# Performance work log

Measured on AMD Instinct MI355X. Metric: run time of the kernel, lower is better.

## Reference

```python
import jax, jax.numpy as jnp
import numpy as np

B, S, E = 512, 200, 128
NUM_C = 1024
DIFF = 100


def _glorot(k, shape):
    fan_in, fan_out = shape[-1], shape[0]
    lim = jnp.sqrt(6.0 / (fan_in + fan_out)).astype(jnp.float32)
    return jax.random.uniform(k, shape, jnp.float32, -lim, lim)


def setup_inputs() -> dict:
    key = jax.random.key(0)
    ks = jax.random.split(key, 16)
    c = jax.random.randint(ks[0], (B, S), 0, NUM_C + 1)
    sd = jax.random.randint(ks[1], (B, S), 0, DIFF + 2)
    a = jax.random.randint(ks[2], (B, S), 0, 2)
    cshft = jax.random.randint(ks[3], (B, S), 0, NUM_C + 1)
    sdshft = jax.random.randint(ks[4], (B, S), 0, DIFF + 2)
    # embedding tables (padding_idx=0 rows zeroed, as in nn.Embedding)
    c_table = _glorot(ks[5], (NUM_C + 1, E)).at[0].set(0.0)
    sd_table = _glorot(ks[6], (DIFF + 2, E)).at[0].set(0.0)
    a_table = _glorot(ks[7], (2, E))
    knowledge = _glorot(ks[8], (1, E))  # xavier_uniform [1, E]
    W1 = _glorot(ks[9], (E, 2 * E)); b1 = jnp.zeros((E,), jnp.float32)
    W2 = _glorot(ks[10], (E, E));     b2 = jnp.zeros((E,), jnp.float32)
    W3 = _glorot(ks[11], (E, E));     b3 = jnp.zeros((E,), jnp.float32)
    W4 = _glorot(ks[12], (E, 2 * E)); b4 = jnp.zeros((E,), jnp.float32)
    W5 = _glorot(ks[13], (E, 2 * E)); b5 = jnp.zeros((E,), jnp.float32)
    W6 = _glorot(ks[14], (E, 3 * E)); b6 = jnp.zeros((E,), jnp.float32)
    return dict(c=c, sd=sd, a=a, cshft=cshft, sdshft=sdshft,
                c_table=c_table, sd_table=sd_table, a_table=a_table,
                knowledge=knowledge,
                W1=W1, b1=b1, W2=W2, b2=b2, W3=W3, b3=b3,
                W4=W4, b4=b4, W5=W5, b5=b5, W6=W6, b6=b6)


def reference(c, sd, a, cshft, sdshft, c_table, sd_table, a_table, knowledge,
              W1, b1, W2, b2, W3, b3, W4, b4, W5, b5, W6, b6):
    # embedding lookups: [B, S, E]
    c_emb = c_table[c]
    sd_emb = sd_table[sd]
    a_emb = a_table[a]
    target_c = c_table[cshft]
    target_sd = sd_table[sdshft]

    input_data = jnp.concatenate((c_emb, sd_emb), -1) @ W1.T + b1      # [B,S,E]
    target_data = jnp.concatenate((target_c, target_sd), -1) @ W1.T + b1

    k0 = jnp.broadcast_to(knowledge, (c.shape[0], knowledge.shape[-1]))  # [B,E]

    def step(k, xs):
        sd_t, a_t, in_t = xs                       # each [B,E]
        qq = k - in_t
        gates_SDF = jax.nn.sigmoid(qq @ W2.T + b2)
        SDFt = gates_SDF * jnp.tanh(qq @ W3.T + b3)  # dropout = eval-mode identity
        x = jnp.concatenate((SDFt, a_t), -1)
        gates_PKA = jax.nn.sigmoid(x @ W4.T + b4)
        PKAt = gates_PKA * jnp.tanh(x @ W5.T + b5)
        ins = jnp.concatenate((k, a_t, sd_t), -1)
        gates_KSU = jax.nn.sigmoid(ins @ W6.T + b6)
        k_new = gates_KSU * k + (1.0 - gates_KSU) * PKAt
        return k_new, k_new

    xs = (jnp.swapaxes(sd_emb, 0, 1),      # [S,B,E]
          jnp.swapaxes(a_emb, 0, 1),
          jnp.swapaxes(input_data, 0, 1))
    _, hs = jax.lax.scan(step, k0, xs)     # hs: [S,B,E]
    output = jnp.swapaxes(hs, 0, 1)        # [B,S,E]

    logits = jnp.sum(target_data * output, axis=-1)  # [B,S]
    return jax.nn.sigmoid(logits)
```

## Files before the change

### kernel.cpp

```cpp
#include <hip/hip_runtime.h>


#define S_ 200
#define E_ 128
#define RS 136

typedef float  float4v __attribute__((ext_vector_type(4)));
typedef _Float16 f16x8 __attribute__((ext_vector_type(8)));

#define BAR() asm volatile("s_waitcnt lgkmcnt(0)\n\ts_barrier" ::: "memory")

#define MFMA(A, B, C) __builtin_amdgcn_mfma_f32_16x16x32_f16((A), (B), (C), 0, 0, 0)

__device__ __forceinline__ float fast_sigmoid(float x) {
  return __builtin_amdgcn_rcpf(1.f + __expf(-x));
}
__device__ __forceinline__ float swz16(float x) {
  return __builtin_bit_cast(float,
      __builtin_amdgcn_ds_swizzle(__builtin_bit_cast(int, x), 0x401F));
}

#define DPP_ADD(x, ctrl) \
  ((x) + __builtin_bit_cast(float, __builtin_amdgcn_update_dpp( \
       0, __builtin_bit_cast(int, (x)), (ctrl), 0xf, 0xf, true)))

__device__ __forceinline__ f16x8 cvt8(const float* __restrict__ p) {
  float4v a = *(const float4v*)p;
  float4v b = *(const float4v*)(p + 4);
  f16x8 r;
  r[0] = (_Float16)a[0]; r[1] = (_Float16)a[1];
  r[2] = (_Float16)a[2]; r[3] = (_Float16)a[3];
  r[4] = (_Float16)b[0]; r[5] = (_Float16)b[1];
  r[6] = (_Float16)b[2]; r[7] = (_Float16)b[3];
  return r;
}

__global__ __launch_bounds__(256) void dimkt_prep(
    const float* __restrict__ c_table, const float* __restrict__ sd_table,
    const float* __restrict__ a_table,
    const float* __restrict__ W1, const float* __restrict__ b1,
    const float* __restrict__ W4, const float* __restrict__ b4,
    const float* __restrict__ W5, const float* __restrict__ b5,
    const float* __restrict__ W6, const float* __restrict__ b6,
    float* __restrict__ ws) {
  __shared__ __attribute__((aligned(16))) float s_src[8][E_];
  __shared__ float s_w[E_][33];
  const int blk = blockIdx.x, t = threadIdx.x;
  const int e = t & 127, h = t >> 7;
  const float* src; const float* wb; const float* bias; float* dst;
  int r0, maxrow, wstr, woff, dstr;
  if (blk < 129)      { r0 = blk * 8;       src = c_table;  maxrow = 1024; wb = W1; wstr = 256; woff = 0;   bias = nullptr; dst = ws;          dstr = 128; }
  else if (blk < 142) { r0 = (blk-129) * 8; src = sd_table; maxrow = 101;  wb = W1; wstr = 256; woff = 128; bias = b1;      dst = ws + 131200; dstr = 256; }
  else if (blk < 155) { r0 = (blk-142) * 8; src = sd_table; maxrow = 101;  wb = W6; wstr = 384; woff = 256; bias = nullptr; dst = ws + 131328; dstr = 256; }
  else if (blk == 155){ r0 = 0;             src = a_table;  maxrow = 1;    wb = W4; wstr = 256; woff = 128; bias = b4;      dst = ws + 157312; dstr = 128; }
  else if (blk == 156){ r0 = 0;             src = a_table;  maxrow = 1;    wb = W5; wstr = 256; woff = 128; bias = b5;      dst = ws + 157568; dstr = 128; }
  else                { r0 = 0;             src = a_table;  maxrow = 1;    wb = W6; wstr = 384; woff = 128; bias = b6;      dst = ws + 157824; dstr = 128; }
  #pragma unroll
  for (int i = 0; i < 4; ++i) {
    int idx = i * 256 + t, row = idx >> 7, col = idx & 127;
    int rr = r0 + row; if (rr > maxrow) rr = maxrow;
    s_src[row][col] = src[rr * E_ + col];
  }
  float binit = bias ? bias[e] : 0.f;
  float acc[4] = {binit, binit, binit, binit};
  for (int k0 = 0; k0 < 4; ++k0) {
    __syncthreads();
    #pragma unroll
    for (int i = 0; i < 16; ++i) {
      int idx = i * 256 + t;
      s_w[idx >> 5][idx & 31] = wb[(idx >> 5) * wstr + woff + k0 * 32 + (idx & 31)];
    }
    __syncthreads();
    #pragma unroll 4
    for (int kk = 0; kk < 32; ++kk) {
      float wv = s_w[e][kk];
      #pragma unroll
      for (int g = 0; g < 4; ++g)
        acc[g] += wv * s_src[h * 4 + g][k0 * 32 + kk];
    }
  }
  #pragma unroll
  for (int g = 0; g < 4; ++g) {
    int row = r0 + h * 4 + g;
    if (row <= maxrow) dst[row * dstr + e] = acc[g];
  }
}

__global__ __launch_bounds__(512, 2) void dimkt_scan(
    const int* __restrict__ c, const int* __restrict__ sd, const int* __restrict__ a,
    const int* __restrict__ cshft, const int* __restrict__ sdshft,
    const float* __restrict__ knowledge,
    const float* __restrict__ W2, const float* __restrict__ b2,
    const float* __restrict__ W3, const float* __restrict__ b3,
    const float* __restrict__ W4, const float* __restrict__ W5,
    const float* __restrict__ W6,
    const float* __restrict__ ws, float* __restrict__ out) {

  const float* __restrict__ C1   = ws;
  const float* __restrict__ SD1I = ws + 131200;
  const float* __restrict__ A4  = ws + 157312;
  const float* __restrict__ A5  = ws + 157568;
  const float* __restrict__ A6  = ws + 157824;

  const int tid  = threadIdx.x;
  const int w    = tid >> 6;
  const int lane = tid & 63;
  const int l15  = lane & 15;
  const int q    = lane >> 4;
  const int qodd = q & 1;
  const int e    = w * 16 + l15;
  const int j    = q >> 1;
  const int bj   = blockIdx.x * 2 + j;

  __shared__ __attribute__((aligned(16))) _Float16 A1[16 * RS];
  __shared__ __attribute__((aligned(16))) _Float16 A2[16 * RS];
  __shared__ __attribute__((aligned(32))) int idx_lds[S_ + 2][2][8];
  __shared__ float part[8][2][S_];

  for (int i = tid; i < 2 * (S_ + 2); i += 512) {
    const int jj = (i >= S_ + 2) ? 1 : 0;
    const int ss = jj ? (i - (S_ + 2)) : i;
    const int sc = ss < S_ ? ss : S_ - 1;
    const int src = (blockIdx.x * 2 + jj) * S_ + sc;
    idx_lds[ss][jj][0] = c[src];
    idx_lds[ss][jj][1] = sd[src];
    idx_lds[ss][jj][2] = a[src];
    idx_lds[ss][jj][3] = cshft[src];
    idx_lds[ss][jj][4] = sdshft[src];
  }

  const int stq = (j * 8) * RS + e;
  const int stk = stq + RS;
  const int rd0 = l15 * RS + q * 8;
  const bool m1 = (l15 & 6) == 0;
  const bool m2 = (l15 & 7) == 0;

  f16x8 w2f[4], w3f[4], w4f[4], w5f[4], w6f[4];
  #pragma unroll
  for (int t = 0; t < 4; ++t) {
    const int ko = t * 32 + q * 8;
    w2f[t] = cvt8(W2 + e * 128 + ko);
    w3f[t] = cvt8(W3 + e * 128 + ko);
    w4f[t] = cvt8(W4 + e * 256 + ko);
    w5f[t] = cvt8(W5 + e * 256 + ko);
    w6f[t] = cvt8(W6 + e * 384 + ko);
  }
  const float b2e = b2[e], b3e = b3[e];
  const float A4t0 = A4[e], A4t1 = A4[E_ + e];
  const float A5t0 = A5[e], A5t1 = A5[E_ + e];
  const float A6t0 = A6[e], A6t1 = A6[E_ + e];

  float kreg = knowledge[e];

  const int base = bj * S_;
  int ic = c[base], isd = sd[base], ia = a[base], ict = cshft[base], ist = sdshft[base];
  float inT0 = C1[ic * E_ + e] + SD1I[isd * 256 + e];
  float sd6v = SD1I[isd * 256 + 128 + e];
  float a4v = ia ? A4t1 : A4t0;
  float a5v = ia ? A5t1 : A5t0;
  float a6v = ia ? A6t1 : A6t0;
  float tgt  = C1[ict * E_ + e] + SD1I[ist * 256 + e];
  float sumPrev = tgt;
  int nic = c[base + 1], nisd = sd[base + 1], nia = a[base + 1],
      nict = cshft[base + 1], nist = sdshft[base + 1];

  __syncthreads();
  if (!qodd) {
    A1[stq] = (_Float16)(kreg - inT0);
    A1[stk] = (_Float16)kreg;
  }
  __syncthreads();

  f16x8 f0{}, f1{}, f2{}, f3{};
  f16x8 g0{}, g1{}, g2v{}, g3{};

  const float4v cin2{b2e, 0.f, 0.f, 0.f};
  const float4v cin3{b3e, 0.f, 0.f, 0.f};
  float4v acc6{0.f,0.f,0.f,0.f};
  float4v acc4{0.f,0.f,0.f,0.f}, acc5{0.f,0.f,0.f,0.f};

  float pprev = 0.f;
  int   sprev = 0;

  #pragma unroll 2
  for (int s = 0; s < S_; ++s) {
    if (m1) {
      f0 = *(const f16x8*)&A1[rd0];
      f1 = *(const f16x8*)&A1[rd0 + 32];
      f2 = *(const f16x8*)&A1[rd0 + 64];
      f3 = *(const f16x8*)&A1[rd0 + 96];
    }

    tgt = swz16(sumPrev);

    const int selc  = qodd ? nict : nic;
    const int selsd = qodd ? nist : nisd;
    const float L1 = C1[selc * E_ + e];
    const float* pSD = SD1I + selsd * 256 + e;
    const float L2   = pSD[0];
    const float nsd6 = pSD[128];
    const float na4 = nia ? A4t1 : A4t0;
    const float na5 = nia ? A5t1 : A5t0;
    const float na6 = nia ? A6t1 : A6t0;

    const int4 iv = *(const int4*)&idx_lds[s + 2][j][0];
    const int tist = idx_lds[s + 2][j][4];

    __builtin_amdgcn_s_setprio(1);
    float4v a2 = MFMA(f0, w2f[0], cin2);
    float4v a3 = MFMA(f0, w3f[0], cin3);
    a2 = MFMA(f1, w2f[1], a2);
    a3 = MFMA(f1, w3f[1], a3);
    a2 = MFMA(f2, w2f[2], a2);
    a3 = MFMA(f2, w3f[2], a3);
    a2 = MFMA(f3, w2f[3], a2);
    a3 = MFMA(f3, w3f[3], a3);

    acc6[1] = a6v + sd6v;
    acc6 = MFMA(f0, w6f[0], acc6);
    acc6 = MFMA(f1, w6f[1], acc6);

    const float g2  = fast_sigmoid(a2[0]);
    const float G2  = g2 + g2;
    const float sg3 = __builtin_amdgcn_rcpf(1.f + __expf(-2.f * a3[0]));
    const float sdfv = G2 * sg3 - g2;
    if (!qodd) A2[stq] = (_Float16)sdfv;

    acc6 = MFMA(f2, w6f[2], acc6);
    acc6 = MFMA(f3, w6f[3], acc6);
    __builtin_amdgcn_s_setprio(0);

    BAR();

    if (m2) {
      g0  = *(const f16x8*)&A2[rd0];
      g1  = *(const f16x8*)&A2[rd0 + 32];
      g2v = *(const f16x8*)&A2[rd0 + 64];
      g3  = *(const f16x8*)&A2[rd0 + 96];
    }

    const float g6 = fast_sigmoid(acc6[1]);
    const float gk = g6 * kreg;
    const float h6 = 1.f - g6;

    if (s > 0) {
      float pr = pprev;
      pr = DPP_ADD(pr, 0x111);
      pr = DPP_ADD(pr, 0x112);
      pr = DPP_ADD(pr, 0x114);
      pr = DPP_ADD(pr, 0x118);
      if (l15 == 15 && !qodd) part[w][j][sprev] = pr;
    }

    __builtin_amdgcn_s_setprio(1);
    acc4[0] = a4v;
    acc4 = MFMA(g0, w4f[0], acc4);
    acc4 = MFMA(g1, w4f[1], acc4);
    acc4 = MFMA(g2v, w4f[2], acc4);
    acc4 = MFMA(g3, w4f[3], acc4);
    acc5[0] = a5v;
    acc5 = MFMA(g0, w5f[0], acc5);
    acc5 = MFMA(g1, w5f[1], acc5);

    const float s4  = fast_sigmoid(acc4[0]);
    const float S42 = s4 + s4;

    acc5 = MFMA(g2v, w5f[2], acc5);
    acc5 = MFMA(g3, w5f[3], acc5);
    __builtin_amdgcn_s_setprio(0);

    const float sg5 = __builtin_amdgcn_rcpf(1.f + __expf(-2.f * acc5[0]));
    const float pka = S42 * sg5 - s4;
    const float knew = pka * h6 + gk;
    kreg = knew;

    const float sum = L1 + L2;

    if (!qodd) {
      A1[stq] = (_Float16)(knew - sum);
      A1[stk] = (_Float16)knew;
    }

    pprev = tgt * knew;
    sprev = s;

    sumPrev = sum;
    sd6v = nsd6; a4v = na4; a5v = na5; a6v = na6;
    nic = iv.x; nisd = iv.y; nia = iv.z; nict = iv.w; nist = tist;

    BAR();
  }

  {
    float pr = pprev;
    pr = DPP_ADD(pr, 0x111);
    pr = DPP_ADD(pr, 0x112);
    pr = DPP_ADD(pr, 0x114);
    pr = DPP_ADD(pr, 0x118);
    if (l15 == 15 && !qodd) part[w][j][sprev] = pr;
  }

  __syncthreads();
  for (int i = tid; i < 2 * S_; i += 512) {
    const int jj = (i >= S_) ? 1 : 0;
    const int ss = jj ? (i - S_) : i;
    float logit = 0.f;
    #pragma unroll
    for (int x = 0; x < 8; ++x) logit += part[x][jj][ss];
    out[(blockIdx.x * 2 + jj) * S_ + ss] = fast_sigmoid(logit);
  }
}

extern "C" void kernel_launch(void* const* d_in, const int* in_sizes, int n_in,
                              void* d_out, int out_size, void* d_ws, size_t ws_size,
                              hipStream_t stream) {
  const int*   c         = (const int*)  d_in[0];
  const int*   sd        = (const int*)  d_in[1];
  const int*   a         = (const int*)  d_in[2];
  const int*   cshft     = (const int*)  d_in[3];
  const int*   sdshft    = (const int*)  d_in[4];
  const float* c_table   = (const float*)d_in[5];
  const float* sd_table  = (const float*)d_in[6];
  const float* a_table   = (const float*)d_in[7];
  const float* knowledge = (const float*)d_in[8];
  const float* W1 = (const float*)d_in[9];  const float* b1 = (const float*)d_in[10];
  const float* W2 = (const float*)d_in[11]; const float* b2 = (const float*)d_in[12];
  const float* W3 = (const float*)d_in[13]; const float* b3 = (const float*)d_in[14];
  const float* W4 = (const float*)d_in[15]; const float* b4 = (const float*)d_in[16];
  const float* W5 = (const float*)d_in[17]; const float* b5 = (const float*)d_in[18];
  const float* W6 = (const float*)d_in[19]; const float* b6 = (const float*)d_in[20];
  float* ws  = (float*)d_ws;
  float* out = (float*)d_out;
  (void)in_sizes; (void)n_in; (void)out_size; (void)ws_size;

  dimkt_prep<<<158, 256, 0, stream>>>(c_table, sd_table, a_table,
                                      W1, b1, W4, b4, W5, b5, W6, b6, ws);
  dimkt_scan<<<256, 512, 0, stream>>>(c, sd, a, cshft, sdshft, knowledge,
                                      W2, b2, W3, b3, W4, W5, W6, ws, out);
}
```

Baseline: 246.6 us.

## Process one batch row per block with 4 waves each owning 32 output features

The scan kernel now handles one sequence per block with 256 threads instead of two sequences with 512 threads. Each wave covers 32 output features using two MFMA tiles per gate, so it holds twice as many weight fragments in registers. The MFMA A-operand rows are duplicated across both 8-row halves. The grid doubles to 512 blocks, which shortens the per-step barriers to 4 waves and spreads work over more CUs. In exchange, each wave has a longer serial MFMA chain per step, higher register pressure, and redundant MFMA work on duplicated rows.

```diff
diff --git a/kernel.cpp b/kernel.cpp
--- a/kernel.cpp
+++ b/kernel.cpp
@@ -86,7 +86,7 @@
   }
 }
 
-__global__ __launch_bounds__(512, 2) void dimkt_scan(
+__global__ __launch_bounds__(256, 2) void dimkt_scan(
     const int* __restrict__ c, const int* __restrict__ sd, const int* __restrict__ a,
     const int* __restrict__ cshft, const int* __restrict__ sdshft,
     const float* __restrict__ knowledge,
@@ -108,42 +108,44 @@
   const int l15  = lane & 15;
   const int q    = lane >> 4;
   const int qodd = q & 1;
-  const int e    = w * 16 + l15;
-  const int j    = q >> 1;
-  const int bj   = blockIdx.x * 2 + j;
+  const int tt   = lane >> 5;
+  const int et0  = w * 32 + l15;
+  const int e    = et0 + tt * 16;
+  const int bj   = blockIdx.x;
 
   __shared__ __attribute__((aligned(16))) _Float16 A1[16 * RS];
   __shared__ __attribute__((aligned(16))) _Float16 A2[16 * RS];
-  __shared__ __attribute__((aligned(32))) int idx_lds[S_ + 2][2][8];
-  __shared__ float part[8][2][S_];
-
-  for (int i = tid; i < 2 * (S_ + 2); i += 512) {
-    const int jj = (i >= S_ + 2) ? 1 : 0;
-    const int ss = jj ? (i - (S_ + 2)) : i;
-    const int sc = ss < S_ ? ss : S_ - 1;
-    const int src = (blockIdx.x * 2 + jj) * S_ + sc;
-    idx_lds[ss][jj][0] = c[src];
-    idx_lds[ss][jj][1] = sd[src];
-    idx_lds[ss][jj][2] = a[src];
-    idx_lds[ss][jj][3] = cshft[src];
-    idx_lds[ss][jj][4] = sdshft[src];
-  }
-
-  const int stq = (j * 8) * RS + e;
-  const int stk = stq + RS;
+  __shared__ __attribute__((aligned(32))) int idx_lds[S_ + 2][8];
+  __shared__ float part[4][2][S_];
+
+  for (int i = tid; i < S_ + 2; i += 256) {
+    const int sc = i < S_ ? i : S_ - 1;
+    const int src = bj * S_ + sc;
+    idx_lds[i][0] = c[src];
+    idx_lds[i][1] = sd[src];
+    idx_lds[i][2] = a[src];
+    idx_lds[i][3] = cshft[src];
+    idx_lds[i][4] = sdshft[src];
+  }
+
   const int rd0 = l15 * RS + q * 8;
   const bool m1 = (l15 & 6) == 0;
   const bool m2 = (l15 & 7) == 0;
 
-  f16x8 w2f[4], w3f[4], w4f[4], w5f[4], w6f[4];
+  f16x8 w2f[2][4], w3f[2][4], w4f[2][4], w5f[2][4], w6f[2][4];
   #pragma unroll
   for (int t = 0; t < 4; ++t) {
     const int ko = t * 32 + q * 8;
-    w2f[t] = cvt8(W2 + e * 128 + ko);
-    w3f[t] = cvt8(W3 + e * 128 + ko);
-    w4f[t] = cvt8(W4 + e * 256 + ko);
-    w5f[t] = cvt8(W5 + e * 256 + ko);
-    w6f[t] = cvt8(W6 + e * 384 + ko);
+    w2f[0][t] = cvt8(W2 + et0 * 128 + ko);
+    w2f[1][t] = cvt8(W2 + (et0 + 16) * 128 + ko);
+    w3f[0][t] = cvt8(W3 + et0 * 128 + ko);
+    w3f[1][t] = cvt8(W3 + (et0 + 16) * 128 + ko);
+    w4f[0][t] = cvt8(W4 + et0 * 256 + ko);
+    w4f[1][t] = cvt8(W4 + (et0 + 16) * 256 + ko);
+    w5f[0][t] = cvt8(W5 + et0 * 256 + ko);
+    w5f[1][t] = cvt8(W5 + (et0 + 16) * 256 + ko);
+    w6f[0][t] = cvt8(W6 + et0 * 384 + ko);
+    w6f[1][t] = cvt8(W6 + (et0 + 16) * 384 + ko);
   }
   const float b2e = b2[e], b3e = b3[e];
   const float A4t0 = A4[e], A4t1 = A4[E_ + e];
@@ -166,23 +168,25 @@
 
   __syncthreads();
   if (!qodd) {
-    A1[stq] = (_Float16)(kreg - inT0);
-    A1[stk] = (_Float16)kreg;
+    const _Float16 hq = (_Float16)(kreg - inT0);
+    const _Float16 hk = (_Float16)kreg;
+    A1[e] = hq;            A1[RS + e] = hk;
+    A1[8 * RS + e] = hq;   A1[9 * RS + e] = hk;
   }
   __syncthreads();
 
   f16x8 f0{}, f1{}, f2{}, f3{};
-  f16x8 g0{}, g1{}, g2v{}, g3{};
 
   const float4v cin2{b2e, 0.f, 0.f, 0.f};
   const float4v cin3{b3e, 0.f, 0.f, 0.f};
-  float4v acc6{0.f,0.f,0.f,0.f};
-  float4v acc4{0.f,0.f,0.f,0.f}, acc5{0.f,0.f,0.f,0.f};
+  float4v acc6a{0.f,0.f,0.f,0.f}, acc6b{0.f,0.f,0.f,0.f};
+  float4v acc4a{0.f,0.f,0.f,0.f}, acc4b{0.f,0.f,0.f,0.f};
+  float4v acc5a{0.f,0.f,0.f,0.f}, acc5b{0.f,0.f,0.f,0.f};
 
   float pprev = 0.f;
   int   sprev = 0;
 
-  #pragma unroll 2
+  #pragma unroll 1
   for (int s = 0; s < S_; ++s) {
     if (m1) {
       f0 = *(const f16x8*)&A1[rd0];
@@ -203,43 +207,64 @@
     const float na5 = nia ? A5t1 : A5t0;
     const float na6 = nia ? A6t1 : A6t0;
 
-    const int4 iv = *(const int4*)&idx_lds[s + 2][j][0];
-    const int tist = idx_lds[s + 2][j][4];
+    const int4 iv = *(const int4*)&idx_lds[s + 2][0];
+    const int tist = idx_lds[s + 2][4];
 
     __builtin_amdgcn_s_setprio(1);
-    float4v a2 = MFMA(f0, w2f[0], cin2);
-    float4v a3 = MFMA(f0, w3f[0], cin3);
-    a2 = MFMA(f1, w2f[1], a2);
-    a3 = MFMA(f1, w3f[1], a3);
-    a2 = MFMA(f2, w2f[2], a2);
-    a3 = MFMA(f2, w3f[2], a3);
-    a2 = MFMA(f3, w2f[3], a2);
-    a3 = MFMA(f3, w3f[3], a3);
-
-    acc6[1] = a6v + sd6v;
-    acc6 = MFMA(f0, w6f[0], acc6);
-    acc6 = MFMA(f1, w6f[1], acc6);
-
-    const float g2  = fast_sigmoid(a2[0]);
+    float4v a2a = MFMA(f0, w2f[0][0], cin2);
+    float4v a3a = MFMA(f0, w3f[0][0], cin3);
+    float4v a2b = MFMA(f0, w2f[1][0], cin2);
+    float4v a3b = MFMA(f0, w3f[1][0], cin3);
+    a2a = MFMA(f1, w2f[0][1], a2a);
+    a3a = MFMA(f1, w3f[0][1], a3a);
+    a2b = MFMA(f1, w2f[1][1], a2b);
+    a3b = MFMA(f1, w3f[1][1], a3b);
+    a2a = MFMA(f2, w2f[0][2], a2a);
+    a3a = MFMA(f2, w3f[0][2], a3a);
+    a2b = MFMA(f2, w2f[1][2], a2b);
+    a3b = MFMA(f2, w3f[1][2], a3b);
+    a2a = MFMA(f3, w2f[0][3], a2a);
+    a3a = MFMA(f3, w3f[0][3], a3a);
+    a2b = MFMA(f3, w2f[1][3], a2b);
+    a3b = MFMA(f3, w3f[1][3], a3b);
+
+    const float bk6 = a6v + sd6v;
+    acc6a[1] = bk6;
+    acc6b[1] = bk6;
+    acc6a = MFMA(f0, w6f[0][0], acc6a);
+    acc6b = MFMA(f0, w6f[1][0], acc6b);
+    acc6a = MFMA(f1, w6f[0][1], acc6a);
+    acc6b = MFMA(f1, w6f[1][1], acc6b);
+
+    const float a2s = tt ? a2b[0] : a2a[0];
+    const float a3s = tt ? a3b[0] : a3a[0];
+    const float g2  = fast_sigmoid(a2s);
     const float G2  = g2 + g2;
-    const float sg3 = __builtin_amdgcn_rcpf(1.f + __expf(-2.f * a3[0]));
+    const float sg3 = __builtin_amdgcn_rcpf(1.f + __expf(-2.f * a3s));
     const float sdfv = G2 * sg3 - g2;
-    if (!qodd) A2[stq] = (_Float16)sdfv;
-
-    acc6 = MFMA(f2, w6f[2], acc6);
-    acc6 = MFMA(f3, w6f[3], acc6);
+    if (!qodd) {
+      const _Float16 hs = (_Float16)sdfv;
+      A2[e] = hs;
+      A2[8 * RS + e] = hs;
+    }
+
+    acc6a = MFMA(f2, w6f[0][2], acc6a);
+    acc6b = MFMA(f2, w6f[1][2], acc6b);
+    acc6a = MFMA(f3, w6f[0][3], acc6a);
+    acc6b = MFMA(f3, w6f[1][3], acc6b);
     __builtin_amdgcn_s_setprio(0);
 
     BAR();
 
     if (m2) {
-      g0  = *(const f16x8*)&A2[rd0];
-      g1  = *(const f16x8*)&A2[rd0 + 32];
-      g2v = *(const f16x8*)&A2[rd0 + 64];
-      g3  = *(const f16x8*)&A2[rd0 + 96];
-    }
-
-    const float g6 = fast_sigmoid(acc6[1]);
+      f0 = *(const f16x8*)&A2[rd0];
+      f1 = *(const f16x8*)&A2[rd0 + 32];
+      f2 = *(const f16x8*)&A2[rd0 + 64];
+      f3 = *(const f16x8*)&A2[rd0 + 96];
+    }
+
+    const float a6s = tt ? acc6b[1] : acc6a[1];
+    const float g6 = fast_sigmoid(a6s);
     const float gk = g6 * kreg;
     const float h6 = 1.f - g6;
 
@@ -249,27 +274,39 @@
       pr = DPP_ADD(pr, 0x112);
       pr = DPP_ADD(pr, 0x114);
       pr = DPP_ADD(pr, 0x118);
-      if (l15 == 15 && !qodd) part[w][j][sprev] = pr;
+      if (l15 == 15 && !qodd) part[w][tt][sprev] = pr;
     }
 
     __builtin_amdgcn_s_setprio(1);
-    acc4[0] = a4v;
-    acc4 = MFMA(g0, w4f[0], acc4);
-    acc4 = MFMA(g1, w4f[1], acc4);
-    acc4 = MFMA(g2v, w4f[2], acc4);
-    acc4 = MFMA(g3, w4f[3], acc4);
-    acc5[0] = a5v;
-    acc5 = MFMA(g0, w5f[0], acc5);
-    acc5 = MFMA(g1, w5f[1], acc5);
-
-    const float s4  = fast_sigmoid(acc4[0]);
+    acc4a[0] = a4v;
+    acc4b[0] = a4v;
+    acc4a = MFMA(f0, w4f[0][0], acc4a);
+    acc4b = MFMA(f0, w4f[1][0], acc4b);
+    acc4a = MFMA(f1, w4f[0][1], acc4a);
+    acc4b = MFMA(f1, w4f[1][1], acc4b);
+    acc4a = MFMA(f2, w4f[0][2], acc4a);
+    acc4b = MFMA(f2, w4f[1][2], acc4b);
+    acc4a = MFMA(f3, w4f[0][3], acc4a);
+    acc4b = MFMA(f3, w4f[1][3], acc4b);
+    acc5a[0] = a5v;
+    acc5b[0] = a5v;
+    acc5a = MFMA(f0, w5f[0][0], acc5a);
+    acc5b = MFMA(f0, w5f[1][0], acc5b);
+    acc5a = MFMA(f1, w5f[0][1], acc5a);
+    acc5b = MFMA(f1, w5f[1][1], acc5b);
+
+    const float a4s = tt ? acc4b[0] : acc4a[0];
+    const float s4  = fast_sigmoid(a4s);
     const float S42 = s4 + s4;
 
-    acc5 = MFMA(g2v, w5f[2], acc5);
-    acc5 = MFMA(g3, w5f[3], acc5);
+    acc5a = MFMA(f2, w5f[0][2], acc5a);
+    acc5b = MFMA(f2, w5f[1][2], acc5b);
+    acc5a = MFMA(f3, w5f[0][3], acc5a);
+    acc5b = MFMA(f3, w5f[1][3], acc5b);
     __builtin_amdgcn_s_setprio(0);
 
-    const float sg5 = __builtin_amdgcn_rcpf(1.f + __expf(-2.f * acc5[0]));
+    const float a5s = tt ? acc5b[0] : acc5a[0];
+    const float sg5 = __builtin_amdgcn_rcpf(1.f + __expf(-2.f * a5s));
     const float pka = S42 * sg5 - s4;
     const float knew = pka * h6 + gk;
     kreg = knew;
@@ -277,8 +314,10 @@
     const float sum = L1 + L2;
 
     if (!qodd) {
-      A1[stq] = (_Float16)(knew - sum);
-      A1[stk] = (_Float16)knew;
+      const _Float16 hq = (_Float16)(knew - sum);
+      const _Float16 hk = (_Float16)knew;
+      A1[e] = hq;            A1[RS + e] = hk;
+      A1[8 * RS + e] = hq;   A1[9 * RS + e] = hk;
     }
 
     pprev = tgt * knew;
@@ -297,17 +336,18 @@
     pr = DPP_ADD(pr, 0x112);
     pr = DPP_ADD(pr, 0x114);
     pr = DPP_ADD(pr, 0x118);
-    if (l15 == 15 && !qodd) part[w][j][sprev] = pr;
+    if (l15 == 15 && !qodd) part[w][tt][sprev] = pr;
   }
 
   __syncthreads();
-  for (int i = tid; i < 2 * S_; i += 512) {
-    const int jj = (i >= S_) ? 1 : 0;
-    const int ss = jj ? (i - S_) : i;
+  for (int i = tid; i < S_; i += 256) {
     float logit = 0.f;
     #pragma unroll
-    for (int x = 0; x < 8; ++x) logit += part[x][jj][ss];
-    out[(blockIdx.x * 2 + jj) * S_ + ss] = fast_sigmoid(logit);
+    for (int x = 0; x < 4; ++x) {
+      logit += part[x][0][i];
+      logit += part[x][1][i];
+    }
+    out[bj * S_ + i] = fast_sigmoid(logit);
   }
 }
 
@@ -335,6 +375,6 @@
 
   dimkt_prep<<<158, 256, 0, stream>>>(c_table, sd_table, a_table,
                                       W1, b1, W4, b4, W5, b5, W6, b6, ws);
-  dimkt_scan<<<256, 512, 0, stream>>>(c, sd, a, cshft, sdshft, knowledge,
+  dimkt_scan<<<512, 256, 0, stream>>>(c, sd, a, cshft, sdshft, knowledge,
                                       W2, b2, W3, b3, W4, W5, W6, ws, out);
 }
```

Measured after the change: 309.2 us. 25.4% more time.
